# Kernel optimization log

Hardware: AMD Instinct MI355X
Metric: run time of the kernel (lower is better)

## Reference

```python
import jax, jax.numpy as jnp
import numpy as np

EPS = 1e-5

def setup_inputs() -> dict:
    key = jax.random.key(0)
    ks = jax.random.split(key, 10)
    B, C, H, W = 4, 512, 56, 56
    n_heads = 8
    nq = H * W
    oq = (H // 2) * (W // 2)  # sr_ratio=2, k=3,s=2,p=1 -> halved spatial dims
    s = 0.02
    return {
        'x': jax.random.normal(ks[0], (B, C, H, W), jnp.float32),
        'attn_weights': jax.random.uniform(ks[1], (B, n_heads, nq, oq), jnp.float32),
        'q_w': jax.random.normal(ks[2], (C, C), jnp.float32) * s,
        'k_w': jax.random.normal(ks[3], (C, C), jnp.float32) * s,
        'v_w': jax.random.normal(ks[4], (C, C), jnp.float32) * s,
        'sr_w': jax.random.normal(ks[5], (C, 1, 3, 3), jnp.float32) * s,  # depthwise OIHW
        'sr_b': jnp.zeros((C,), jnp.float32),
        'ln_g': jnp.ones((C,), jnp.float32),
        'ln_b': jnp.zeros((C,), jnp.float32),
        'tc_w': jax.random.normal(ks[6], (n_heads, n_heads), jnp.float32) * 0.3,  # 1x1 conv over heads
        'tc_b': jnp.zeros((n_heads,), jnp.float32),
        'proj_w': jax.random.normal(ks[7], (C, C), jnp.float32) * s,
        'proj_b': jnp.zeros((C,), jnp.float32),
    }

def _layernorm(x, g, b):
    m = jnp.mean(x, axis=-1, keepdims=True)
    v = jnp.var(x, axis=-1, keepdims=True)
    return (x - m) * jax.lax.rsqrt(v + EPS) * g + b

def reference(x, attn_weights, q_w, k_w, v_w, sr_w, sr_b, ln_g, ln_b, tc_w, tc_b, proj_w, proj_b):
    B, C, H, W = x.shape
    n_heads = tc_w.shape[0]
    hd = C // n_heads
    scale = hd ** -0.5
    nq = H * W
    xf = x.reshape(B, C, nq).transpose(0, 2, 1)  # (B, nq, C)
    q = (xf @ q_w.T).reshape(B, nq, n_heads, hd).transpose(0, 2, 1, 3)  # (B, h, nq, hd)
    # spatial reduction: depthwise conv k=3, s=2, p=1 on NCHW, then LayerNorm
    xs = jax.lax.conv_general_dilated(
        x, sr_w, window_strides=(2, 2), padding=((1, 1), (1, 1)),
        feature_group_count=C, dimension_numbers=('NCHW', 'OIHW', 'NCHW'))
    xs = xs + sr_b[None, :, None, None]
    oq = xs.shape[2] * xs.shape[3]
    xs = xs.reshape(B, C, oq).transpose(0, 2, 1)  # (B, oq, C)
    xs = _layernorm(xs, ln_g, ln_b)
    k = (xs @ k_w.T).reshape(B, oq, n_heads, hd).transpose(0, 2, 3, 1)  # (B, h, hd, oq)
    v = (xs @ v_w.T).reshape(B, oq, n_heads, hd).transpose(0, 2, 1, 3)  # (B, h, oq, hd)
    attn = jnp.einsum('bhqd,bhdo->bhqo', q, k) * scale  # (B, h, nq, oq)
    # apply_transform: 1x1 conv mixing heads -> softmax -> InstanceNorm2d (no affine)
    attn = jnp.einsum('bhqo,gh->bgqo', attn, tc_w) + tc_b[None, :, None, None]
    attn = jax.nn.softmax(attn, axis=-1)
    m = jnp.mean(attn, axis=(2, 3), keepdims=True)
    var = jnp.var(attn, axis=(2, 3), keepdims=True)
    attn = (attn - m) * jax.lax.rsqrt(var + EPS)
    attn = attn_weights * attn
    out = jnp.einsum('bhqo,bhod->bhqd', attn, v)  # (B, h, nq, hd)
    out = out.transpose(0, 2, 1, 3).reshape(B, nq, C)
    out = out @ proj_w.T + proj_b
    return out.reshape(B, H, W, C).transpose(0, 3, 1, 2)
```

## Files before the change

kernel.cpp:

```cpp
#include <hip/hip_runtime.h>

typedef _Float16 half8 __attribute__((ext_vector_type(8)));
typedef _Float16 half4 __attribute__((ext_vector_type(4)));
typedef float fx4 __attribute__((ext_vector_type(4)));

#define MFMA16(a,b,c) __builtin_amdgcn_mfma_f32_16x16x32_f16(a,b,c,0,0,0)

#define BN 4
#define CC 512
#define HH 56
#define WW 56
#define NQ 3136
#define OQ 784
#define NH 8
#define HD 64
#define NSEG 7
#define BGN (BN * NH * NQ)

__device__ inline half8 h8z() {
    half8 v;
#pragma unroll
    for (int j = 0; j < 8; j++) v[j] = (_Float16)0.f;
    return v;
}

__global__ void cvt4_kernel(const float* __restrict__ a, const float* __restrict__ b,
                            const float* __restrict__ c, const float* __restrict__ d,
                            _Float16* __restrict__ o, float* __restrict__ S2) {
    if (blockIdx.x == 0 && blockIdx.y == 0 && threadIdx.x < 32) S2[threadIdx.x] = 0.f;
    int y = blockIdx.y;
    const float* s = (y == 0) ? a : (y == 1) ? b : (y == 2) ? c : d;
    int i = blockIdx.x * 256 + threadIdx.x;
    o[(size_t)y * 262144 + i] = (_Float16)s[i];
}

__global__ void xpose_kernel(const float* __restrict__ x, _Float16* __restrict__ xf) {
    __shared__ float t[32][33];
    int n0 = blockIdx.x * 32, c0 = blockIdx.y * 32, b = blockIdx.z;
    int tx = threadIdx.x, ty = threadIdx.y;
#pragma unroll
    for (int i = 0; i < 4; i++)
        t[ty + 8 * i][tx] = x[((size_t)(b * CC) + c0 + ty + 8 * i) * NQ + n0 + tx];
    __syncthreads();
#pragma unroll
    for (int i = 0; i < 4; i++)
        xf[((size_t)(b * NQ) + n0 + ty + 8 * i) * CC + c0 + tx] = (_Float16)t[tx][ty + 8 * i];
}

__global__ void dw_kernel(const float* __restrict__ x, const float* __restrict__ w,
                          const float* __restrict__ bias, float* __restrict__ xsc) {
    int cb = blockIdx.x, oy = blockIdx.y, b = blockIdx.z;
    int tx = threadIdx.x, ty = threadIdx.y;
    int c = cb * 16 + ty;
    float a = bias[c];
    const float* xp = x + ((size_t)(b * CC + c) * HH) * WW;
#pragma unroll
    for (int ky = 0; ky < 3; ky++) {
        int iy = 2 * oy - 1 + ky;
        if (iy < 0 || iy >= HH) continue;
#pragma unroll
        for (int kx = 0; kx < 3; kx++) {
            int ix = 2 * tx - 1 + kx;
            if (ix < 0 || ix >= WW) continue;
            a += xp[iy * WW + ix] * w[c * 9 + ky * 3 + kx];
        }
    }
    __shared__ float tile[28][17];
    tile[tx][ty] = a;
    __syncthreads();
    int lin = ty * 28 + tx;
    int oi = lin >> 4, ci = lin & 15;
    xsc[((size_t)(b * OQ) + oy * 28 + oi) * CC + cb * 16 + ci] = tile[oi][ci];
}

__global__ __launch_bounds__(256) void ln_kernel(const float* __restrict__ xsc,
        const float* __restrict__ g, const float* __restrict__ bb,
        _Float16* __restrict__ xs16) {
    int row = blockIdx.x;
    const float* rp = xsc + (size_t)row * CC;
    int t = threadIdx.x;
    float v0 = rp[t], v1 = rp[t + 256];
    float s = v0 + v1, ss = v0 * v0 + v1 * v1;
#pragma unroll
    for (int m = 1; m < 64; m <<= 1) {
        s += __shfl_xor(s, m, 64);
        ss += __shfl_xor(ss, m, 64);
    }
    __shared__ float red[8];
    int wv = t >> 6;
    if ((t & 63) == 0) { red[wv] = s; red[4 + wv] = ss; }
    __syncthreads();
    s = red[0] + red[1] + red[2] + red[3];
    ss = red[4] + red[5] + red[6] + red[7];
    float mean = s * (1.f / 512.f);
    float var = ss * (1.f / 512.f) - mean * mean;
    float rs = rsqrtf(var + 1e-5f);
    xs16[(size_t)row * CC + t] = (_Float16)((v0 - mean) * rs * g[t] + bb[t]);
    xs16[(size_t)row * CC + t + 256] = (_Float16)((v1 - mean) * rs * g[t + 256] + bb[t + 256]);
}

__global__ __launch_bounds__(256) void gemm_qkv(const _Float16* __restrict__ xf,
        const _Float16* __restrict__ xs, const _Float16* __restrict__ w4,
        _Float16* __restrict__ q16, _Float16* __restrict__ k16, _Float16* __restrict__ vT) {
    const int which = blockIdx.z;
    if (which && blockIdx.x >= 49) return;
    const _Float16* A = which ? xs : xf;
    const _Float16* Bw = w4 + (size_t)which * 262144;
    __shared__ _Float16 As[64 * 72];
    __shared__ _Float16 Bs[64 * 72];
    const int m0 = blockIdx.x * 64, n0 = blockIdx.y * 64;
    const int tid = threadIdx.x;
    const int lane = tid & 63, wv = tid >> 6;
    const int wm = (wv >> 1) * 32, wn = (wv & 1) * 32;
    const int l15 = lane & 15, quad = lane >> 4;
    fx4 acc[2][2];
#pragma unroll
    for (int i = 0; i < 2; i++)
#pragma unroll
        for (int j = 0; j < 2; j++) acc[i][j] = fx4{0.f, 0.f, 0.f, 0.f};
    for (int k0 = 0; k0 < 512; k0 += 64) {
        __syncthreads();
#pragma unroll
        for (int i = 0; i < 2; i++) {
            int id = tid + 256 * i;
            int r = id >> 3, kc = (id & 7) << 3;
            *(half8*)(As + r * 72 + kc) = *(const half8*)(A + (size_t)(m0 + r) * 512 + k0 + kc);
            *(half8*)(Bs + r * 72 + kc) = *(const half8*)(Bw + (size_t)(n0 + r) * 512 + k0 + kc);
        }
        __syncthreads();
#pragma unroll
        for (int ks = 0; ks < 2; ks++) {
            half8 af[2], bf[2];
#pragma unroll
            for (int s = 0; s < 2; s++) {
                af[s] = *(const half8*)(As + (wm + s * 16 + l15) * 72 + ks * 32 + quad * 8);
                bf[s] = *(const half8*)(Bs + (wn + s * 16 + l15) * 72 + ks * 32 + quad * 8);
            }
#pragma unroll
            for (int i = 0; i < 2; i++)
#pragma unroll
                for (int j = 0; j < 2; j++)
                    acc[i][j] = MFMA16(af[i], bf[j], acc[i][j]);
        }
    }
    if (which < 2) {
        _Float16* O = which ? k16 : q16;
#pragma unroll
        for (int i = 0; i < 2; i++)
#pragma unroll
            for (int j = 0; j < 2; j++) {
                int col = n0 + wn + j * 16 + l15;
#pragma unroll
                for (int e = 0; e < 4; e++) {
                    int row = m0 + wm + i * 16 + quad * 4 + e;
                    O[(size_t)row * 512 + col] = (_Float16)acc[i][j][e];
                }
            }
    } else {
#pragma unroll
        for (int i = 0; i < 2; i++) {
            int row = m0 + wm + i * 16 + quad * 4;
            int b = row / OQ;
            int o = row - b * OQ;
#pragma unroll
            for (int j = 0; j < 2; j++) {
                int c = n0 + wn + j * 16 + l15;
                half4 pk;
#pragma unroll
                for (int e = 0; e < 4; e++) pk[e] = (_Float16)acc[i][j][e];
                *(half4*)(vT + ((size_t)(b * NH + (c >> 6)) * HD + (c & 63)) * OQ + o) = pk;
            }
        }
    }
}

__global__ __launch_bounds__(256) void qk_mix(const _Float16* __restrict__ q16,
        const _Float16* __restrict__ k16, const float* __restrict__ tcw,
        const float* __restrict__ tcb, _Float16* __restrict__ L,
        float* __restrict__ Zpart, float* __restrict__ E2part) {
    __shared__ _Float16 kl[16 * 520];
    __shared__ float tcs[64];
    __shared__ float tbb[8];
    const int b = blockIdx.z, oseg = blockIdx.y, ob = oseg * 112;
    const int tid = threadIdx.x;
    const int wv = tid >> 6, lane = tid & 63, l15 = lane & 15, quad = lane >> 4;
    const int n0 = blockIdx.x * 64 + wv * 16;
    if (tid < 64) tcs[tid] = tcw[tid] * 0.125f;
    else if (tid < 72) tbb[tid - 64] = tcb[tid - 64];

    half8 aF[8][2];
    const _Float16* qrow = q16 + ((size_t)(b * NQ + n0 + l15)) * 512;
#pragma unroll
    for (int h = 0; h < 8; h++)
#pragma unroll
        for (int ks = 0; ks < 2; ks++)
            aF[h][ks] = *(const half8*)(qrow + h * 64 + ks * 32 + quad * 8);

    float z[8][4], s2[8][4];
#pragma unroll
    for (int g = 0; g < 8; g++)
#pragma unroll
        for (int e = 0; e < 4; e++) { z[g][e] = 0.f; s2[g][e] = 0.f; }

    for (int ot = 0; ot < 7; ot++) {
        int o0 = ob + ot * 16;
        __syncthreads();
        const _Float16* kb = k16 + ((size_t)(b * OQ + o0)) * 512;
#pragma unroll
        for (int i = 0; i < 4; i++) {
            int id = tid + 256 * i;
            int r = id >> 6, c = (id & 63) << 3;
            *(half8*)(kl + r * 520 + c) = *(const half8*)(kb + (size_t)r * 512 + c);
        }
        __syncthreads();
        fx4 s[8];
#pragma unroll
        for (int h = 0; h < 8; h++) {
            fx4 a = fx4{0.f, 0.f, 0.f, 0.f};
#pragma unroll
            for (int ks = 0; ks < 2; ks++) {
                half8 bF = *(const half8*)(kl + l15 * 520 + h * 64 + ks * 32 + quad * 8);
                a = MFMA16(aF[h][ks], bF, a);
            }
            s[h] = a;
        }
#pragma unroll
        for (int g = 0; g < 8; g++) {
#pragma unroll
            for (int e = 0; e < 4; e++) {
                float v = tbb[g];
#pragma unroll
                for (int h = 0; h < 8; h++) v += tcs[g * 8 + h] * s[h][e];
                _Float16 vh = (_Float16)v;
                float vr = (float)vh;
                float ex = __expf(vr);
                z[g][e] += ex;
                s2[g][e] += ex * ex;
                L[((size_t)((b * 8 + g) * NQ) + n0 + quad * 4 + e) * OQ + o0 + l15] = vh;
            }
        }
    }
#pragma unroll
    for (int m = 1; m < 16; m <<= 1) {
#pragma unroll
        for (int g = 0; g < 8; g++)
#pragma unroll
            for (int e = 0; e < 4; e++) {
                z[g][e] += __shfl_xor(z[g][e], m, 64);
                s2[g][e] += __shfl_xor(s2[g][e], m, 64);
            }
    }
    if (l15 < 8) {
        int g = l15;
        size_t base = (size_t)oseg * BGN + (size_t)(b * 8 + g) * NQ + n0 + quad * 4;
#pragma unroll
        for (int e = 0; e < 4; e++) {
            Zpart[base + e] = z[g][e];
            E2part[base + e] = s2[g][e];
        }
    }
}

__global__ __launch_bounds__(256) void zfin_kernel(const float* __restrict__ Zpart,
        const float* __restrict__ E2part, float* __restrict__ Zinv, float* __restrict__ S2) {
    int i = blockIdx.x * 256 + threadIdx.x;
    float z = 0.f, e2 = 0.f;
#pragma unroll
    for (int s = 0; s < NSEG; s++) {
        z += Zpart[(size_t)s * BGN + i];
        e2 += E2part[(size_t)s * BGN + i];
    }
    float zi = 1.f / z;
    Zinv[i] = zi;
    float r = e2 * zi * zi;
#pragma unroll
    for (int m = 1; m < 64; m <<= 1) r += __shfl_xor(r, m, 64);
    if ((threadIdx.x & 63) == 0) atomicAdd(&S2[i / NQ], r);
}

__global__ __launch_bounds__(256) void pv_kernel(const _Float16* __restrict__ L,
        const float* __restrict__ W, const _Float16* __restrict__ vT,
        const float* __restrict__ Zinv, const float* __restrict__ S2,
        _Float16* __restrict__ outp) {
    const int b = blockIdx.z, g = blockIdx.y;
    const int tid = threadIdx.x;
    const int wv = tid >> 6, lane = tid & 63, l15 = lane & 15, quad = lane >> 4;
    const int n0 = blockIdx.x * 64 + wv * 16;
    const int bg = b * 8 + g;
    const float mm = 1.f / (float)OQ;
    const float rv = rsqrtf(S2[bg] * (1.f / ((float)NQ * (float)OQ)) - mm * mm + 1e-5f);
    const float czr = Zinv[bg * NQ + n0 + l15] * rv;
    const float rm = rv * mm;
    const _Float16* Lrow = L + ((size_t)bg * NQ + n0 + l15) * OQ;
    const float* Wrow = W + ((size_t)bg * NQ + n0 + l15) * OQ;
    const _Float16* vb = vT + (size_t)bg * HD * OQ + (size_t)l15 * OQ;

    half8 aL, bL;
    fx4 aW0, aW1, bW0, bW1;
    half8 aV0, aV1, aV2, aV3, bV0, bV1, bV2, bV3;

#define LOADC(c, dL, dW0, dW1, dV0, dV1, dV2, dV3)                          \
    {                                                                        \
        int kb = (c) * 32 + quad * 8;                                        \
        if (kb < OQ) {                                                       \
            dL = *(const half8*)(Lrow + kb);                                 \
            dW0 = *(const fx4*)(Wrow + kb);                                  \
            dW1 = *(const fx4*)(Wrow + kb + 4);                              \
            dV0 = *(const half8*)(vb + (size_t)(0 * 16) * OQ + kb);          \
            dV1 = *(const half8*)(vb + (size_t)(1 * 16) * OQ + kb);          \
            dV2 = *(const half8*)(vb + (size_t)(2 * 16) * OQ + kb);          \
            dV3 = *(const half8*)(vb + (size_t)(3 * 16) * OQ + kb);          \
        } else {                                                             \
            dL = h8z();                                                      \
            dW0 = fx4{0.f, 0.f, 0.f, 0.f};                                   \
            dW1 = fx4{0.f, 0.f, 0.f, 0.f};                                   \
            dV0 = h8z(); dV1 = h8z(); dV2 = h8z(); dV3 = h8z();              \
        }                                                                    \
    }

    fx4 acc0 = fx4{0.f, 0.f, 0.f, 0.f};
    fx4 acc1 = fx4{0.f, 0.f, 0.f, 0.f};
    fx4 acc2 = fx4{0.f, 0.f, 0.f, 0.f};
    fx4 acc3 = fx4{0.f, 0.f, 0.f, 0.f};

#define COMPUTE(sL, sW0, sW1, sV0, sV1, sV2, sV3)                            \
    {                                                                        \
        half8 aH;                                                            \
        _Pragma("unroll")                                                    \
        for (int j = 0; j < 8; j++) {                                        \
            float e = __expf((float)sL[j]);                                  \
            float a = e * czr - rm;                                          \
            float wx = (j < 4) ? sW0[j] : sW1[j - 4];                        \
            aH[j] = (_Float16)(a * wx);                                      \
        }                                                                    \
        acc0 = MFMA16(aH, sV0, acc0);                                        \
        acc1 = MFMA16(aH, sV1, acc1);                                        \
        acc2 = MFMA16(aH, sV2, acc2);                                        \
        acc3 = MFMA16(aH, sV3, acc3);                                        \
    }

    LOADC(0, aL, aW0, aW1, aV0, aV1, aV2, aV3);
    for (int oc = 0; oc < 24; oc += 2) {
        LOADC(oc + 1, bL, bW0, bW1, bV0, bV1, bV2, bV3);
        COMPUTE(aL, aW0, aW1, aV0, aV1, aV2, aV3);
        LOADC(oc + 2, aL, aW0, aW1, aV0, aV1, aV2, aV3);
        COMPUTE(bL, bW0, bW1, bV0, bV1, bV2, bV3);
    }
    COMPUTE(aL, aW0, aW1, aV0, aV1, aV2, aV3);

#undef LOADC
#undef COMPUTE

    fx4 acc[4] = {acc0, acc1, acc2, acc3};
#pragma unroll
    for (int ds = 0; ds < 4; ds++)
#pragma unroll
        for (int e = 0; e < 4; e++) {
            int n = n0 + quad * 4 + e;
            int c = g * 64 + ds * 16 + l15;
            outp[((size_t)b * NQ + n) * 512 + c] = (_Float16)acc[ds][e];
        }
}

__global__ __launch_bounds__(256) void gemm_proj(const _Float16* __restrict__ A,
        const _Float16* __restrict__ Ball, const float* __restrict__ bias,
        float* __restrict__ Oall) {
    __shared__ _Float16 As[64 * 72];
    __shared__ _Float16 Bs[64 * 72];
    const int b = blockIdx.z;
    const _Float16* Bm = Ball + (size_t)b * NQ * 512;
    float* O = Oall + (size_t)b * CC * NQ;
    const int m0 = blockIdx.x * 64, n0 = blockIdx.y * 64;
    const int tid = threadIdx.x;
    const int lane = tid & 63, wv = tid >> 6;
    const int wm = (wv >> 1) * 32, wn = (wv & 1) * 32;
    const int l15 = lane & 15, quad = lane >> 4;
    fx4 acc[2][2];
#pragma unroll
    for (int i = 0; i < 2; i++)
#pragma unroll
        for (int j = 0; j < 2; j++) acc[i][j] = fx4{0.f, 0.f, 0.f, 0.f};
    for (int k0 = 0; k0 < 512; k0 += 64) {
        __syncthreads();
#pragma unroll
        for (int i = 0; i < 2; i++) {
            int id = tid + 256 * i;
            int r = id >> 3, kc = (id & 7) << 3;
            *(half8*)(As + r * 72 + kc) = *(const half8*)(A + (size_t)(m0 + r) * 512 + k0 + kc);
            *(half8*)(Bs + r * 72 + kc) = *(const half8*)(Bm + (size_t)(n0 + r) * 512 + k0 + kc);
        }
        __syncthreads();
#pragma unroll
        for (int ks = 0; ks < 2; ks++) {
            half8 af[2], bf[2];
#pragma unroll
            for (int s = 0; s < 2; s++) {
                af[s] = *(const half8*)(As + (wm + s * 16 + l15) * 72 + ks * 32 + quad * 8);
                bf[s] = *(const half8*)(Bs + (wn + s * 16 + l15) * 72 + ks * 32 + quad * 8);
            }
#pragma unroll
            for (int i = 0; i < 2; i++)
#pragma unroll
                for (int j = 0; j < 2; j++)
                    acc[i][j] = MFMA16(af[i], bf[j], acc[i][j]);
        }
    }
#pragma unroll
    for (int i = 0; i < 2; i++)
#pragma unroll
        for (int j = 0; j < 2; j++) {
            int col = n0 + wn + j * 16 + l15;
#pragma unroll
            for (int e = 0; e < 4; e++) {
                int row = m0 + wm + i * 16 + quad * 4 + e;
                O[(size_t)row * NQ + col] = acc[i][j][e] + bias[row];
            }
        }
}

extern "C" void kernel_launch(void* const* d_in, const int* in_sizes, int n_in,
                              void* d_out, int out_size, void* d_ws, size_t ws_size,
                              hipStream_t stream) {
    const float* x = (const float*)d_in[0];
    const float* aw = (const float*)d_in[1];
    const float* q_w = (const float*)d_in[2];
    const float* k_w = (const float*)d_in[3];
    const float* v_w = (const float*)d_in[4];
    const float* sr_w = (const float*)d_in[5];
    const float* sr_b = (const float*)d_in[6];
    const float* ln_g = (const float*)d_in[7];
    const float* ln_b = (const float*)d_in[8];
    const float* tc_w = (const float*)d_in[9];
    const float* tc_b = (const float*)d_in[10];
    const float* p_w = (const float*)d_in[11];
    const float* p_b = (const float*)d_in[12];
    float* out = (float*)d_out;

    char* p = (char*)d_ws;
    auto take = [&](size_t bytes) -> char* {
        char* r = p;
        p += (bytes + 255) & ~(size_t)255;
        return r;
    };
    _Float16* qw16 = (_Float16*)take(512 * 512 * 2);
    _Float16* kw16 = (_Float16*)take(512 * 512 * 2);
    _Float16* vw16 = (_Float16*)take(512 * 512 * 2);
    _Float16* pw16 = (_Float16*)take(512 * 512 * 2);
    _Float16* xf16 = (_Float16*)take((size_t)BN * NQ * CC * 2);
    float* xsc = (float*)take((size_t)BN * OQ * CC * 4);
    _Float16* xs16 = (_Float16*)take((size_t)BN * OQ * CC * 2);
    _Float16* q16 = (_Float16*)take((size_t)BN * NQ * CC * 2);
    _Float16* k16 = (_Float16*)take((size_t)BN * OQ * CC * 2);
    _Float16* vT = (_Float16*)take((size_t)BN * OQ * CC * 2);
    _Float16* outp = (_Float16*)take((size_t)BN * NQ * CC * 2);
    float* Zpart = (float*)take((size_t)NSEG * BGN * 4);
    float* E2part = (float*)take((size_t)NSEG * BGN * 4);
    float* S2 = (float*)take(32 * 4);
    float* Zinv = (float*)take((size_t)BGN * 4);
    _Float16* L = (_Float16*)take((size_t)BN * NH * NQ * OQ * 2);

    cvt4_kernel<<<dim3(1024, 4), 256, 0, stream>>>(q_w, k_w, v_w, p_w, qw16, S2);
    xpose_kernel<<<dim3(98, 16, BN), dim3(32, 8), 0, stream>>>(x, xf16);
    dw_kernel<<<dim3(32, 28, BN), dim3(28, 16), 0, stream>>>(x, sr_w, sr_b, xsc);
    ln_kernel<<<BN * OQ, 256, 0, stream>>>(xsc, ln_g, ln_b, xs16);
    gemm_qkv<<<dim3(196, 8, 3), 256, 0, stream>>>(xf16, xs16, qw16, q16, k16, vT);
    qk_mix<<<dim3(49, 7, BN), 256, 0, stream>>>(q16, k16, tc_w, tc_b, L, Zpart, E2part);
    zfin_kernel<<<BGN / 256, 256, 0, stream>>>(Zpart, E2part, Zinv, S2);
    pv_kernel<<<dim3(49, 8, BN), 256, 0, stream>>>(L, aw, vT, Zinv, S2, outp);
    gemm_proj<<<dim3(8, 49, BN), 256, 0, stream>>>(pw16, outp, p_b, out);
}
```

Before: 765.8 us.

## Tile logit buffer for coalesced loads and stage attn weights via LDS in PV

```diff
diff --git a/kernel.cpp b/kernel.cpp
--- a/kernel.cpp
+++ b/kernel.cpp
@@ -226,6 +226,8 @@
         }
 #pragma unroll
         for (int g = 0; g < 8; g++) {
+            size_t tb = (((size_t)(b * 8 + g) * 196 + (n0 >> 4)) * 49 + (o0 >> 4)) * 256
+                        + (l15 >> 3) * 128 + (l15 & 7);
 #pragma unroll
             for (int e = 0; e < 4; e++) {
                 float v = tbb[g];
@@ -236,7 +238,7 @@
                 float ex = __expf(vr);
                 z[g][e] += ex;
                 s2[g][e] += ex * ex;
-                L[((size_t)((b * 8 + g) * NQ) + n0 + quad * 4 + e) * OQ + o0 + l15] = vh;
+                L[tb + (quad * 4 + e) * 8] = vh;
             }
         }
     }
@@ -278,10 +280,11 @@
     if ((threadIdx.x & 63) == 0) atomicAdd(&S2[i / NQ], r);
 }
 
-__global__ __launch_bounds__(256) void pv_kernel(const _Float16* __restrict__ L,
+__global__ __launch_bounds__(256) void pv_kernel(const _Float16* __restrict__ Lt,
         const float* __restrict__ W, const _Float16* __restrict__ vT,
         const float* __restrict__ Zinv, const float* __restrict__ S2,
         _Float16* __restrict__ outp) {
+    __shared__ float Ws[4][2][16 * 70];
     const int b = blockIdx.z, g = blockIdx.y;
     const int tid = threadIdx.x;
     const int wv = tid >> 6, lane = tid & 63, l15 = lane & 15, quad = lane >> 4;
@@ -291,65 +294,105 @@
     const float rv = rsqrtf(S2[bg] * (1.f / ((float)NQ * (float)OQ)) - mm * mm + 1e-5f);
     const float czr = Zinv[bg * NQ + n0 + l15] * rv;
     const float rm = rv * mm;
-    const _Float16* Lrow = L + ((size_t)bg * NQ + n0 + l15) * OQ;
+    const _Float16* Lb = Lt + (((size_t)bg * 196 + (n0 >> 4)) * 49) * 256 + lane * 8;
+    const float* Wg = W + ((size_t)bg * NQ + n0 + (lane >> 4)) * OQ + (lane & 15) * 4;
     const float* Wrow = W + ((size_t)bg * NQ + n0 + l15) * OQ;
     const _Float16* vb = vT + (size_t)bg * HD * OQ + (size_t)l15 * OQ;
-
-    half8 aL, bL;
-    fx4 aW0, aW1, bW0, bW1;
-    half8 aV0, aV1, aV2, aV3, bV0, bV1, bV2, bV3;
-
-#define LOADC(c, dL, dW0, dW1, dV0, dV1, dV2, dV3)                          \
-    {                                                                        \
-        int kb = (c) * 32 + quad * 8;                                        \
-        if (kb < OQ) {                                                       \
-            dL = *(const half8*)(Lrow + kb);                                 \
-            dW0 = *(const fx4*)(Wrow + kb);                                  \
-            dW1 = *(const fx4*)(Wrow + kb + 4);                              \
-            dV0 = *(const half8*)(vb + (size_t)(0 * 16) * OQ + kb);          \
-            dV1 = *(const half8*)(vb + (size_t)(1 * 16) * OQ + kb);          \
-            dV2 = *(const half8*)(vb + (size_t)(2 * 16) * OQ + kb);          \
-            dV3 = *(const half8*)(vb + (size_t)(3 * 16) * OQ + kb);          \
-        } else {                                                             \
-            dL = h8z();                                                      \
-            dW0 = fx4{0.f, 0.f, 0.f, 0.f};                                   \
-            dW1 = fx4{0.f, 0.f, 0.f, 0.f};                                   \
-            dV0 = h8z(); dV1 = h8z(); dV2 = h8z(); dV3 = h8z();              \
-        }                                                                    \
-    }
-
+    float* WsW = &Ws[wv][0][0];
+    const float* WsR = &Ws[wv][0][0] + l15 * 70 + quad * 8;
+
+    fx4 wreg[4];
+    half8 lA, lB, vA0, vA1, vA2, vA3, vB0, vB1, vB2, vB3;
     fx4 acc0 = fx4{0.f, 0.f, 0.f, 0.f};
     fx4 acc1 = fx4{0.f, 0.f, 0.f, 0.f};
     fx4 acc2 = fx4{0.f, 0.f, 0.f, 0.f};
     fx4 acc3 = fx4{0.f, 0.f, 0.f, 0.f};
 
-#define COMPUTE(sL, sW0, sW1, sV0, sV1, sV2, sV3)                            \
+#define LOADWG(g2)                                                           \
+    {                                                                        \
+        _Pragma("unroll") for (int i = 0; i < 4; i++)                        \
+            wreg[i] = *(const fx4*)(Wg + (size_t)(4 * i) * OQ + (g2) * 64);  \
+    }
+#define DSWR(ph)                                                             \
+    {                                                                        \
+        _Pragma("unroll") for (int i = 0; i < 4; i++)                        \
+            *(fx4*)(WsW + (ph) * (16 * 70) + ((lane >> 4) + 4 * i) * 70 +    \
+                    (lane & 15) * 4) = wreg[i];                              \
+    }
+#define LOADL(c, d)                                                          \
+    {                                                                        \
+        if ((c) < 24 || lane < 32) d = *(const half8*)(Lb + (c) * 512);      \
+        else d = h8z();                                                      \
+    }
+#define LOADV(c, d0, d1, d2, d3)                                             \
+    {                                                                        \
+        int kb = (c) * 32 + quad * 8;                                        \
+        if (kb < OQ) {                                                       \
+            d0 = *(const half8*)(vb + (size_t)(0 * 16) * OQ + kb);           \
+            d1 = *(const half8*)(vb + (size_t)(1 * 16) * OQ + kb);           \
+            d2 = *(const half8*)(vb + (size_t)(2 * 16) * OQ + kb);           \
+            d3 = *(const half8*)(vb + (size_t)(3 * 16) * OQ + kb);           \
+        } else { d0 = h8z(); d1 = h8z(); d2 = h8z(); d3 = h8z(); }           \
+    }
+#define COMPUTE_W(sL, wf0, wf1, s0, s1, s2, s3)                              \
     {                                                                        \
         half8 aH;                                                            \
-        _Pragma("unroll")                                                    \
-        for (int j = 0; j < 8; j++) {                                        \
+        _Pragma("unroll") for (int j = 0; j < 8; j++) {                      \
             float e = __expf((float)sL[j]);                                  \
             float a = e * czr - rm;                                          \
-            float wx = (j < 4) ? sW0[j] : sW1[j - 4];                        \
+            float wx = (j < 4) ? wf0[j] : wf1[j - 4];                        \
             aH[j] = (_Float16)(a * wx);                                      \
         }                                                                    \
-        acc0 = MFMA16(aH, sV0, acc0);                                        \
-        acc1 = MFMA16(aH, sV1, acc1);                                        \
-        acc2 = MFMA16(aH, sV2, acc2);                                        \
-        acc3 = MFMA16(aH, sV3, acc3);                                        \
-    }
-
-    LOADC(0, aL, aW0, aW1, aV0, aV1, aV2, aV3);
-    for (int oc = 0; oc < 24; oc += 2) {
-        LOADC(oc + 1, bL, bW0, bW1, bV0, bV1, bV2, bV3);
-        COMPUTE(aL, aW0, aW1, aV0, aV1, aV2, aV3);
-        LOADC(oc + 2, aL, aW0, aW1, aV0, aV1, aV2, aV3);
-        COMPUTE(bL, bW0, bW1, bV0, bV1, bV2, bV3);
-    }
-    COMPUTE(aL, aW0, aW1, aV0, aV1, aV2, aV3);
-
-#undef LOADC
-#undef COMPUTE
+        acc0 = MFMA16(aH, s0, acc0);                                         \
+        acc1 = MFMA16(aH, s1, acc1);                                         \
+        acc2 = MFMA16(aH, s2, acc2);                                         \
+        acc3 = MFMA16(aH, s3, acc3);                                         \
+    }
+
+    LOADWG(0);
+    LOADL(0, lA);
+    LOADV(0, vA0, vA1, vA2, vA3);
+    DSWR(0);
+    LOADWG(1);
+
+#pragma unroll 1
+    for (int pi = 0; pi < 12; ++pi) {
+        const int phC = pi & 1, phN = phC ^ 1;
+        if (pi <= 10) DSWR(phN);
+        if (pi <= 9) LOADWG(pi + 2);
+        const int c0 = 2 * pi;
+        LOADL(c0 + 1, lB);
+        LOADV(c0 + 1, vB0, vB1, vB2, vB3);
+        {
+            const float* wr = WsR + phC * (16 * 70);
+            fx4 wf0 = *(const fx4*)(wr);
+            fx4 wf1 = *(const fx4*)(wr + 4);
+            COMPUTE_W(lA, wf0, wf1, vA0, vA1, vA2, vA3);
+        }
+        LOADL(c0 + 2, lA);
+        LOADV(c0 + 2, vA0, vA1, vA2, vA3);
+        {
+            const float* wr = WsR + phC * (16 * 70) + 32;
+            fx4 wf0 = *(const fx4*)(wr);
+            fx4 wf1 = *(const fx4*)(wr + 4);
+            COMPUTE_W(lB, wf0, wf1, vB0, vB1, vB2, vB3);
+        }
+    }
+    {
+        fx4 wt0 = fx4{0.f, 0.f, 0.f, 0.f};
+        fx4 wt1 = fx4{0.f, 0.f, 0.f, 0.f};
+        int kb = 768 + quad * 8;
+        if (kb < OQ) {
+            wt0 = *(const fx4*)(Wrow + kb);
+            wt1 = *(const fx4*)(Wrow + kb + 4);
+        }
+        COMPUTE_W(lA, wt0, wt1, vA0, vA1, vA2, vA3);
+    }
+#undef LOADWG
+#undef DSWR
+#undef LOADL
+#undef LOADV
+#undef COMPUTE_W
 
     fx4 acc[4] = {acc0, acc1, acc2, acc3};
 #pragma unroll
```

After: 706.5 us. 1.08x faster.
